# Optimization experiments

Measured on AMD Instinct MI355X. Metric: run time of the kernel, lower is better.

## Reference

```python
import jax, jax.numpy as jnp
import numpy as np

BS, N, D_IN, D_OUT = 4, 512, 64, 64
TEMP = 1.0
POOL_K = 0.5
N_KEEP = max(int(N * POOL_K), 1)  # 256
BN_EPS = 1e-5


def setup_inputs() -> dict:
    key = jax.random.key(0)
    ks = jax.random.split(key, 12)
    xav = lambda k, shape: jax.random.normal(k, shape, jnp.float32) * np.sqrt(2.0 / sum(shape))
    return {
        "x": jax.random.normal(ks[0], (BS, N, D_IN), jnp.float32),
        "att_proj_w": xav(ks[1], (D_IN, D_OUT)),
        "att_proj_b": jnp.zeros((D_OUT,), jnp.float32),
        "att_weight": xav(ks[2], (D_OUT, 1))[:, 0],  # (D_OUT,)
        "pwa_w": xav(ks[3], (D_IN, D_OUT)),
        "pwa_b": jnp.zeros((D_OUT,), jnp.float32),
        "pwoa_w": xav(ks[4], (D_IN, D_OUT)),
        "pwoa_b": jnp.zeros((D_OUT,), jnp.float32),
        "bn_gamma": jnp.ones((D_OUT,), jnp.float32),
        "bn_beta": jnp.zeros((D_OUT,), jnp.float32),
        "bn_mean": jnp.zeros((D_OUT,), jnp.float32),
        "bn_var": jnp.ones((D_OUT,), jnp.float32),
        "pool_w": xav(ks[5], (D_OUT, 1))[:, 0],  # (D_OUT,)
        "pool_b": jnp.zeros((), jnp.float32),
    }


def reference(x, att_proj_w, att_proj_b, att_weight, pwa_w, pwa_b,
              pwoa_w, pwoa_b, bn_gamma, bn_beta, bn_mean, bn_var,
              pool_w, pool_b):
    # ---- GraphAttentionLayer (eval mode: dropout off, BN uses running stats) ----
    # pairwise node product: (bs, i, j, d)
    pair = x[:, :, None, :] * x[:, None, :, :]
    a = jnp.tanh(jnp.einsum('bijd,de->bije', pair, att_proj_w) + att_proj_b)
    scores = jnp.einsum('bije,e->bij', a, att_weight) / TEMP
    att = jax.nn.softmax(scores, axis=-1)  # torch softmax over dim=-2 of (bs,i,j,1) == j axis
    agg = jnp.einsum('bij,bjd->bid', att, x)
    h = (agg @ pwa_w + pwa_b) + (x @ pwoa_w + pwoa_b)
    h = (h - bn_mean) * jax.lax.rsqrt(bn_var + BN_EPS) * bn_gamma + bn_beta
    h = jax.nn.selu(h)
    # ---- GraphPool (eval: dropout off) ----
    s = jax.nn.sigmoid(h @ pool_w + pool_b)  # (bs, N)
    _, idx = jax.lax.top_k(s, N_KEEP)        # (bs, N_KEEP), sorted desc like torch.topk
    hs = h * s[..., None]
    out = jnp.take_along_axis(hs, idx[..., None], axis=1)  # (bs, N_KEEP, D_OUT)
    return out
```

## Files before the change

### kernel.cpp

```cpp
#include <hip/hip_runtime.h>
#include <hip/hip_bf16.h>
#include <math.h>

#define BSZ 4
#define NN 512
#define DD 64
#define NKEEP 256

typedef __attribute__((ext_vector_type(8))) short short8;
typedef __attribute__((ext_vector_type(4))) float f32x4;

__device__ __forceinline__ ushort f2bf_rne(float f) {
  union { float f; unsigned u; } v; v.f = f;
  unsigned r = v.u + 0x7fffu + ((v.u >> 16) & 1u);
  return (ushort)(r >> 16);
}
__device__ __forceinline__ float bf2f(ushort h) {
  union { unsigned u; float f; } v; v.u = ((unsigned)h) << 16;
  return v.f;
}
__device__ __forceinline__ void split2t(float a, float b, uint& hu, uint& lu) {
  const uint au = __float_as_uint(a), bu = __float_as_uint(b);
  hu = (au >> 16) | (bu & 0xffff0000u);
  const float ra = a - __uint_as_float(au & 0xffff0000u);
  const float rb = b - __uint_as_float(bu & 0xffff0000u);
  lu = (__float_as_uint(ra) >> 16) | (__float_as_uint(rb) & 0xffff0000u);
}

__global__ void k_prep(const float* __restrict__ apw,
                       ushort* __restrict__ wht, ushort* __restrict__ wlt,
                       int* __restrict__ tile_tab) {
  const int idx = blockIdx.x * 256 + threadIdx.x;
  const int d = idx >> 6, e = idx & 63;
  const float wv = apw[idx];
  const ushort h = f2bf_rne(wv);
  const ushort lo = f2bf_rne(wv - bf2f(h));
  wht[e * 64 + d] = h;
  wlt[e * 64 + d] = lo;
  if (idx < 1056) {
    int it = 0, rem = idx;
    while (rem >= 32 - (it >> 1)) { rem -= 32 - (it >> 1); ++it; }
    const int jt = (it >> 1) + rem;
    tile_tab[idx] = it | (jt << 8);
  }
}

__global__ __launch_bounds__(256) void k_score(
    const float* __restrict__ x, const ushort* __restrict__ wht,
    const ushort* __restrict__ wlt, const float* __restrict__ apb,
    const float* __restrict__ aw, const int* __restrict__ tile_tab,
    float* __restrict__ sT) {
  __shared__ __align__(16) float T[4][8][16];

  const int w = threadIdx.x >> 6;
  const int l = threadIdx.x & 63;
  const int il = l & 15, g = l >> 4;
  const int task = blockIdx.x * 4 + w;
  const int b = task / 1056;
  const int pid = task - b * 1056;
  const int pk = tile_tab[pid];
  const int it = pk & 0xff, jt = pk >> 8;
  const int i0 = it * 8, j0 = jt * 16;
  const bool diag = ((it >> 1) == jt);

  const float* xb = x + (size_t)b * NN * DD;
  float* plane = sT + (size_t)b * NN * NN;

  short8 wfh[4][2], wfl[4][2];
  #pragma unroll
  for (int eq = 0; eq < 4; ++eq)
    #pragma unroll
    for (int ks = 0; ks < 2; ++ks) {
      const int off = (eq * 16 + il) * 64 + ks * 32 + g * 8;
      wfh[eq][ks] = *reinterpret_cast<const short8*>(wht + off);
      wfl[eq][ks] = *reinterpret_cast<const short8*>(wlt + off);
    }

  const float K2 = 2.8853900817779268f;
  float aw2_4[4], bK2[4], awq = 0.f;
  #pragma unroll
  for (int eq = 0; eq < 4; ++eq) {
    const float a = aw[eq * 16 + il];
    aw2_4[eq] = 2.f * a;
    bK2[eq] = apb[eq * 16 + il] * K2;
    awq += a;
  }
  awq += __shfl_xor(awq, 1, 64);
  awq += __shfl_xor(awq, 2, 64);
  awq += __shfl_xor(awq, 4, 64);
  awq += __shfl_xor(awq, 8, 64);
  const float awC = awq;

  const float* xjr = xb + (size_t)(j0 + il) * DD;
  const float4 xj0 = *reinterpret_cast<const float4*>(xjr + g * 8);
  const float4 xj1 = *reinterpret_cast<const float4*>(xjr + g * 8 + 4);
  const float4 xj2 = *reinterpret_cast<const float4*>(xjr + 32 + g * 8);
  const float4 xj3 = *reinterpret_cast<const float4*>(xjr + 32 + g * 8 + 4);

  const float* xir0 = xb + (size_t)i0 * DD;
  float4 nx0 = *reinterpret_cast<const float4*>(xir0 + g * 8);
  float4 nx1 = *reinterpret_cast<const float4*>(xir0 + g * 8 + 4);
  float4 nx2 = *reinterpret_cast<const float4*>(xir0 + 32 + g * 8);
  float4 nx3 = *reinterpret_cast<const float4*>(xir0 + 32 + g * 8 + 4);

  #pragma unroll 2
  for (int ii = 0; ii < 8; ++ii) {
    const int i_glob = i0 + ii;
    const float4 xi0 = nx0, xi1 = nx1, xi2 = nx2, xi3 = nx3;
    if (ii < 7) {
      const float* xirn = xb + (size_t)(i_glob + 1) * DD;
      nx0 = *reinterpret_cast<const float4*>(xirn + g * 8);
      nx1 = *reinterpret_cast<const float4*>(xirn + g * 8 + 4);
      nx2 = *reinterpret_cast<const float4*>(xirn + 32 + g * 8);
      nx3 = *reinterpret_cast<const float4*>(xirn + 32 + g * 8 + 4);
    }

    union { uint u[4]; short8 s; } hA, lA, hB, lB;
    split2t(xj0.x * xi0.x, xj0.y * xi0.y, hA.u[0], lA.u[0]);
    split2t(xj0.z * xi0.z, xj0.w * xi0.w, hA.u[1], lA.u[1]);
    split2t(xj1.x * xi1.x, xj1.y * xi1.y, hA.u[2], lA.u[2]);
    split2t(xj1.z * xi1.z, xj1.w * xi1.w, hA.u[3], lA.u[3]);
    split2t(xj2.x * xi2.x, xj2.y * xi2.y, hB.u[0], lB.u[0]);
    split2t(xj2.z * xi2.z, xj2.w * xi2.w, hB.u[1], lB.u[1]);
    split2t(xj3.x * xi3.x, xj3.y * xi3.y, hB.u[2], lB.u[2]);
    split2t(xj3.z * xi3.z, xj3.w * xi3.w, hB.u[3], lB.u[3]);

    f32x4 acc[4];
    #pragma unroll
    for (int eq = 0; eq < 4; ++eq) acc[eq] = (f32x4){0.f, 0.f, 0.f, 0.f};
    #pragma unroll
    for (int eq = 0; eq < 4; ++eq) {
      acc[eq] = __builtin_amdgcn_mfma_f32_16x16x32_bf16(hA.s, wfh[eq][0], acc[eq], 0, 0, 0);
      acc[eq] = __builtin_amdgcn_mfma_f32_16x16x32_bf16(hA.s, wfl[eq][0], acc[eq], 0, 0, 0);
      acc[eq] = __builtin_amdgcn_mfma_f32_16x16x32_bf16(lA.s, wfh[eq][0], acc[eq], 0, 0, 0);
      acc[eq] = __builtin_amdgcn_mfma_f32_16x16x32_bf16(hB.s, wfh[eq][1], acc[eq], 0, 0, 0);
      acc[eq] = __builtin_amdgcn_mfma_f32_16x16x32_bf16(hB.s, wfl[eq][1], acc[eq], 0, 0, 0);
      acc[eq] = __builtin_amdgcn_mfma_f32_16x16x32_bf16(lB.s, wfh[eq][1], acc[eq], 0, 0, 0);
    }

    float neg[4] = {0.f, 0.f, 0.f, 0.f};
    #pragma unroll
    for (int eq = 0; eq < 4; ++eq)
      #pragma unroll
      for (int rr = 0; rr < 4; ++rr) {
        const float ex = __builtin_amdgcn_exp2f(fmaf(acc[eq][rr], K2, bK2[eq]));
        const float rc = __builtin_amdgcn_rcpf(ex + 1.0f);
        neg[rr] = fmaf(aw2_4[eq], rc, neg[rr]);
      }
    #pragma unroll
    for (int rr = 0; rr < 4; ++rr) {
      neg[rr] += __shfl_xor(neg[rr], 1, 64);
      neg[rr] += __shfl_xor(neg[rr], 2, 64);
      neg[rr] += __shfl_xor(neg[rr], 4, 64);
      neg[rr] += __shfl_xor(neg[rr], 8, 64);
    }
    const f32x4 sc = {awC - neg[0], awC - neg[1], awC - neg[2], awC - neg[3]};

    if (il == 0) {
      if (!diag) {
        *reinterpret_cast<f32x4*>(plane + (size_t)i_glob * NN + j0 + g * 4) = sc;
      } else {
        #pragma unroll
        for (int rr = 0; rr < 4; ++rr) {
          const int jv = j0 + g * 4 + rr;
          if (jv >= i_glob) plane[(size_t)i_glob * NN + jv] = sc[rr];
        }
      }
      *reinterpret_cast<f32x4*>(&T[w][ii][g * 4]) = sc;
    }
  }

  __syncthreads();

  {
    const int jv = l >> 2;
    const int ip = (l & 3) * 2;
    const float m0 = T[w][ip + 0][jv];
    const float m1 = T[w][ip + 1][jv];
    const int jr = j0 + jv;
    if (!diag) {
      const float2 mv = {m0, m1};
      *reinterpret_cast<float2*>(plane + (size_t)jr * NN + i0 + ip) = mv;
    } else {
      if (jr > i0 + ip + 0) plane[(size_t)jr * NN + i0 + ip + 0] = m0;
      if (jr > i0 + ip + 1) plane[(size_t)jr * NN + i0 + ip + 1] = m1;
    }
  }
}

__global__ __launch_bounds__(256) void k_soft(
    const float* __restrict__ x, const float* __restrict__ sT,
    const float* __restrict__ pwa, const float* __restrict__ pwab,
    const float* __restrict__ pwoa, const float* __restrict__ pwob,
    const float* __restrict__ gam, const float* __restrict__ bet,
    const float* __restrict__ mu, const float* __restrict__ var,
    const float* __restrict__ poolw, const float* __restrict__ poolb,
    float* __restrict__ h, float* __restrict__ s) {
  __shared__ float ssc[2][512];
  __shared__ float srm[2][4], srs[2][4];
  __shared__ float sagg[4][2][64];
  __shared__ float rag[2][64], xis[2][64];

  const int t = threadIdx.x;
  const int w = t >> 6, l = t & 63;
  const int b = blockIdx.x >> 8;
  const int rp = blockIdx.x & 255;
  const int i_r0 = rp * 2, i_r1 = i_r0 + 1;
  const float* xb = x + (size_t)b * NN * DD;
  const float* pl0 = sT + (size_t)b * NN * NN;
  const int jw = w * 128;

  const size_t o0 = (size_t)i_r0 * NN + jw + l;
  const size_t o1 = (size_t)i_r1 * NN + jw + l;
  float r0a = pl0[o0];
  float r0b = pl0[o0 + 64];
  float r1a = pl0[o1];
  float r1b = pl0[o1 + 64];
  float m0 = fmaxf(r0a, r0b), m1 = fmaxf(r1a, r1b);
  #pragma unroll
  for (int off = 32; off; off >>= 1) {
    m0 = fmaxf(m0, __shfl_xor(m0, off, 64));
    m1 = fmaxf(m1, __shfl_xor(m1, off, 64));
  }
  if (l == 0) { srm[0][w] = m0; srm[1][w] = m1; }
  __syncthreads();
  m0 = fmaxf(fmaxf(srm[0][0], srm[0][1]), fmaxf(srm[0][2], srm[0][3]));
  m1 = fmaxf(fmaxf(srm[1][0], srm[1][1]), fmaxf(srm[1][2], srm[1][3]));

  const float L2E = 1.4426950408889634f;
  float e0a = __builtin_amdgcn_exp2f((r0a - m0) * L2E);
  float e0b = __builtin_amdgcn_exp2f((r0b - m0) * L2E);
  float e1a = __builtin_amdgcn_exp2f((r1a - m1) * L2E);
  float e1b = __builtin_amdgcn_exp2f((r1b - m1) * L2E);
  float ps0 = e0a + e0b, ps1 = e1a + e1b;
  #pragma unroll
  for (int off = 32; off; off >>= 1) {
    ps0 += __shfl_xor(ps0, off, 64);
    ps1 += __shfl_xor(ps1, off, 64);
  }
  if (l == 0) { srs[0][w] = ps0; srs[1][w] = ps1; }
  __syncthreads();
  const float inv0 = 1.f / (srs[0][0] + srs[0][1] + srs[0][2] + srs[0][3]);
  const float inv1 = 1.f / (srs[1][0] + srs[1][1] + srs[1][2] + srs[1][3]);
  ssc[0][jw + l] = e0a * inv0;
  ssc[0][jw + 64 + l] = e0b * inv0;
  ssc[1][jw + l] = e1a * inv1;
  ssc[1][jw + 64 + l] = e1b * inv1;
  __syncthreads();

  float g0a = 0.f, g0b = 0.f, g1a = 0.f, g1b = 0.f;
  #pragma unroll 4
  for (int jj = 0; jj < 128; jj += 2) {
    const int j = jw + jj;
    const float xv0 = xb[(size_t)j * DD + l];
    const float xv1 = xb[(size_t)(j + 1) * DD + l];
    g0a = fmaf(ssc[0][j], xv0, g0a);
    g1a = fmaf(ssc[1][j], xv0, g1a);
    g0b = fmaf(ssc[0][j + 1], xv1, g0b);
    g1b = fmaf(ssc[1][j + 1], xv1, g1b);
  }
  sagg[w][0][l] = g0a + g0b;
  sagg[w][1][l] = g1a + g1b;
  __syncthreads();

  if (w < 2) {
    const int irow = i_r0 + w;
    rag[w][l] = sagg[0][w][l] + sagg[1][w][l] + sagg[2][w][l] + sagg[3][w][l];
    xis[w][l] = xb[(size_t)irow * DD + l];
    float acc = 0.f;
    #pragma unroll 8
    for (int d = 0; d < 64; ++d) {
      acc = fmaf(rag[w][d], pwa[d * 64 + l], acc);
      acc = fmaf(xis[w][d], pwoa[d * 64 + l], acc);
    }
    acc += pwab[l] + pwob[l];
    float hb = (acc - mu[l]) * rsqrtf(var[l] + 1e-5f) * gam[l] + bet[l];
    const float SC = 1.0507009873554805f, AL = 1.6732632423543772f;
    float hv = hb > 0.f ? SC * hb : SC * AL * expm1f(hb);
    h[((size_t)(b * NN + irow)) * DD + l] = hv;

    float p = hv * poolw[l];
    #pragma unroll
    for (int off = 32; off; off >>= 1) p += __shfl_xor(p, off, 64);
    if (l == 0) s[b * NN + irow] = 1.f / (1.f + expf(-(p + poolb[0])));
  }
}

__global__ __launch_bounds__(512) void k_sel(
    const float* __restrict__ s, const float* __restrict__ h,
    float* __restrict__ out) {
  __shared__ float svv[NN];
  __shared__ int inv[NKEEP];
  __shared__ float sval[NKEEP];
  const int b = blockIdx.x, t = threadIdx.x;
  svv[t] = s[b * NN + t];
  __syncthreads();

  const float my = svv[t];
  int r = 0;
  #pragma unroll 4
  for (int j0 = 0; j0 < NN; j0 += 4) {
    float4 v = *reinterpret_cast<const float4*>(&svv[j0]);
    r += (v.x > my) || (v.x == my && (j0 + 0) < t);
    r += (v.y > my) || (v.y == my && (j0 + 1) < t);
    r += (v.z > my) || (v.z == my && (j0 + 2) < t);
    r += (v.w > my) || (v.w == my && (j0 + 3) < t);
  }
  if (r < NKEEP) { inv[r] = t; sval[r] = my; }
  __syncthreads();

  #pragma unroll
  for (int pos = t; pos < NKEEP * 16; pos += 512) {
    const int kk = pos >> 4, d4 = (pos & 15) * 4;
    const int i = inv[kk];
    const float sc = sval[kk];
    float4 v = *reinterpret_cast<const float4*>(
        h + ((size_t)(b * NN + i)) * DD + d4);
    v.x *= sc; v.y *= sc; v.z *= sc; v.w *= sc;
    *reinterpret_cast<float4*>(out + ((size_t)(b * NKEEP + kk)) * DD + d4) = v;
  }
}

extern "C" void kernel_launch(void* const* d_in, const int* in_sizes, int n_in,
                              void* d_out, int out_size, void* d_ws, size_t ws_size,
                              hipStream_t stream) {
  const float* x     = (const float*)d_in[0];
  const float* apw   = (const float*)d_in[1];
  const float* apb   = (const float*)d_in[2];
  const float* aw    = (const float*)d_in[3];
  const float* pwa   = (const float*)d_in[4];
  const float* pwab  = (const float*)d_in[5];
  const float* pwoa  = (const float*)d_in[6];
  const float* pwob  = (const float*)d_in[7];
  const float* gam   = (const float*)d_in[8];
  const float* bet   = (const float*)d_in[9];
  const float* mu    = (const float*)d_in[10];
  const float* var   = (const float*)d_in[11];
  const float* poolw = (const float*)d_in[12];
  const float* poolb = (const float*)d_in[13];
  float* out = (float*)d_out;

  float* sT    = (float*)d_ws;
  float* h     = sT + (size_t)BSZ * NN * NN;
  float* s     = h + (size_t)BSZ * NN * DD;
  ushort* wht  = (ushort*)(s + BSZ * NN);
  ushort* wlt  = wht + 4096;
  int* tile_tab = (int*)(wlt + 4096);

  k_prep<<<16, 256, 0, stream>>>(apw, wht, wlt, tile_tab);
  k_score<<<1056, 256, 0, stream>>>(x, wht, wlt, apb, aw, tile_tab, sT);
  k_soft<<<BSZ * 256, 256, 0, stream>>>(x, sT, pwa, pwab, pwoa, pwob,
                                        gam, bet, mu, var, poolw, poolb, h, s);
  k_sel<<<BSZ, 512, 0, stream>>>(s, h, out);
}
```

Before: 73.71 us.

## Fold weight prep into score kernel and make score/softmax kernels persistent

Removes the separate prep kernel: each wave now splits the attention projection weights into bf16 hi/lo fragments itself and derives its triangular tile coordinates inline. Both k_score and k_soft become persistent grids of 512 blocks that loop over tasks. This drops one launch and the workspace round-trip for the prepped weights. In exchange it halves resident parallelism, adds per-wave scalar weight loads and conversion, and removes the next-row x prefetch.

New measurement: 67.02 us. -9.1%, faster.

```diff
diff --git a/kernel.cpp b/kernel.cpp
--- a/kernel.cpp
+++ b/kernel.cpp
@@ -27,53 +27,31 @@
   lu = (__float_as_uint(ra) >> 16) | (__float_as_uint(rb) & 0xffff0000u);
 }
 
-__global__ void k_prep(const float* __restrict__ apw,
-                       ushort* __restrict__ wht, ushort* __restrict__ wlt,
-                       int* __restrict__ tile_tab) {
-  const int idx = blockIdx.x * 256 + threadIdx.x;
-  const int d = idx >> 6, e = idx & 63;
-  const float wv = apw[idx];
-  const ushort h = f2bf_rne(wv);
-  const ushort lo = f2bf_rne(wv - bf2f(h));
-  wht[e * 64 + d] = h;
-  wlt[e * 64 + d] = lo;
-  if (idx < 1056) {
-    int it = 0, rem = idx;
-    while (rem >= 32 - (it >> 1)) { rem -= 32 - (it >> 1); ++it; }
-    const int jt = (it >> 1) + rem;
-    tile_tab[idx] = it | (jt << 8);
-  }
-}
-
 __global__ __launch_bounds__(256) void k_score(
-    const float* __restrict__ x, const ushort* __restrict__ wht,
-    const ushort* __restrict__ wlt, const float* __restrict__ apb,
-    const float* __restrict__ aw, const int* __restrict__ tile_tab,
+    const float* __restrict__ x, const float* __restrict__ apw,
+    const float* __restrict__ apb, const float* __restrict__ aw,
     float* __restrict__ sT) {
   __shared__ __align__(16) float T[4][8][16];
 
   const int w = threadIdx.x >> 6;
   const int l = threadIdx.x & 63;
   const int il = l & 15, g = l >> 4;
-  const int task = blockIdx.x * 4 + w;
-  const int b = task / 1056;
-  const int pid = task - b * 1056;
-  const int pk = tile_tab[pid];
-  const int it = pk & 0xff, jt = pk >> 8;
-  const int i0 = it * 8, j0 = jt * 16;
-  const bool diag = ((it >> 1) == jt);
-
-  const float* xb = x + (size_t)b * NN * DD;
-  float* plane = sT + (size_t)b * NN * NN;
 
   short8 wfh[4][2], wfl[4][2];
   #pragma unroll
   for (int eq = 0; eq < 4; ++eq)
     #pragma unroll
     for (int ks = 0; ks < 2; ++ks) {
-      const int off = (eq * 16 + il) * 64 + ks * 32 + g * 8;
-      wfh[eq][ks] = *reinterpret_cast<const short8*>(wht + off);
-      wfl[eq][ks] = *reinterpret_cast<const short8*>(wlt + off);
+      short8 hh, ll;
+      #pragma unroll
+      for (int q = 0; q < 8; ++q) {
+        const int d = ks * 32 + g * 8 + q;
+        const float wv = apw[d * 64 + eq * 16 + il];
+        const ushort h = f2bf_rne(wv);
+        hh[q] = (short)h;
+        ll[q] = (short)f2bf_rne(wv - bf2f(h));
+      }
+      wfh[eq][ks] = hh; wfl[eq][ks] = ll;
     }
 
   const float K2 = 2.8853900817779268f;
@@ -91,99 +69,103 @@
   awq += __shfl_xor(awq, 8, 64);
   const float awC = awq;
 
-  const float* xjr = xb + (size_t)(j0 + il) * DD;
-  const float4 xj0 = *reinterpret_cast<const float4*>(xjr + g * 8);
-  const float4 xj1 = *reinterpret_cast<const float4*>(xjr + g * 8 + 4);
-  const float4 xj2 = *reinterpret_cast<const float4*>(xjr + 32 + g * 8);
-  const float4 xj3 = *reinterpret_cast<const float4*>(xjr + 32 + g * 8 + 4);
-
-  const float* xir0 = xb + (size_t)i0 * DD;
-  float4 nx0 = *reinterpret_cast<const float4*>(xir0 + g * 8);
-  float4 nx1 = *reinterpret_cast<const float4*>(xir0 + g * 8 + 4);
-  float4 nx2 = *reinterpret_cast<const float4*>(xir0 + 32 + g * 8);
-  float4 nx3 = *reinterpret_cast<const float4*>(xir0 + 32 + g * 8 + 4);
-
-  #pragma unroll 2
-  for (int ii = 0; ii < 8; ++ii) {
-    const int i_glob = i0 + ii;
-    const float4 xi0 = nx0, xi1 = nx1, xi2 = nx2, xi3 = nx3;
-    if (ii < 7) {
-      const float* xirn = xb + (size_t)(i_glob + 1) * DD;
-      nx0 = *reinterpret_cast<const float4*>(xirn + g * 8);
-      nx1 = *reinterpret_cast<const float4*>(xirn + g * 8 + 4);
-      nx2 = *reinterpret_cast<const float4*>(xirn + 32 + g * 8);
-      nx3 = *reinterpret_cast<const float4*>(xirn + 32 + g * 8 + 4);
-    }
-
-    union { uint u[4]; short8 s; } hA, lA, hB, lB;
-    split2t(xj0.x * xi0.x, xj0.y * xi0.y, hA.u[0], lA.u[0]);
-    split2t(xj0.z * xi0.z, xj0.w * xi0.w, hA.u[1], lA.u[1]);
-    split2t(xj1.x * xi1.x, xj1.y * xi1.y, hA.u[2], lA.u[2]);
-    split2t(xj1.z * xi1.z, xj1.w * xi1.w, hA.u[3], lA.u[3]);
-    split2t(xj2.x * xi2.x, xj2.y * xi2.y, hB.u[0], lB.u[0]);
-    split2t(xj2.z * xi2.z, xj2.w * xi2.w, hB.u[1], lB.u[1]);
-    split2t(xj3.x * xi3.x, xj3.y * xi3.y, hB.u[2], lB.u[2]);
-    split2t(xj3.z * xi3.z, xj3.w * xi3.w, hB.u[3], lB.u[3]);
-
-    f32x4 acc[4];
-    #pragma unroll
-    for (int eq = 0; eq < 4; ++eq) acc[eq] = (f32x4){0.f, 0.f, 0.f, 0.f};
-    #pragma unroll
-    for (int eq = 0; eq < 4; ++eq) {
-      acc[eq] = __builtin_amdgcn_mfma_f32_16x16x32_bf16(hA.s, wfh[eq][0], acc[eq], 0, 0, 0);
-      acc[eq] = __builtin_amdgcn_mfma_f32_16x16x32_bf16(hA.s, wfl[eq][0], acc[eq], 0, 0, 0);
-      acc[eq] = __builtin_amdgcn_mfma_f32_16x16x32_bf16(lA.s, wfh[eq][0], acc[eq], 0, 0, 0);
-      acc[eq] = __builtin_amdgcn_mfma_f32_16x16x32_bf16(hB.s, wfh[eq][1], acc[eq], 0, 0, 0);
-      acc[eq] = __builtin_amdgcn_mfma_f32_16x16x32_bf16(hB.s, wfl[eq][1], acc[eq], 0, 0, 0);
-      acc[eq] = __builtin_amdgcn_mfma_f32_16x16x32_bf16(lB.s, wfh[eq][1], acc[eq], 0, 0, 0);
-    }
-
-    float neg[4] = {0.f, 0.f, 0.f, 0.f};
-    #pragma unroll
-    for (int eq = 0; eq < 4; ++eq)
-      #pragma unroll
-      for (int rr = 0; rr < 4; ++rr) {
-        const float ex = __builtin_amdgcn_exp2f(fmaf(acc[eq][rr], K2, bK2[eq]));
-        const float rc = __builtin_amdgcn_rcpf(ex + 1.0f);
-        neg[rr] = fmaf(aw2_4[eq], rc, neg[rr]);
-      }
-    #pragma unroll
-    for (int rr = 0; rr < 4; ++rr) {
-      neg[rr] += __shfl_xor(neg[rr], 1, 64);
-      neg[rr] += __shfl_xor(neg[rr], 2, 64);
-      neg[rr] += __shfl_xor(neg[rr], 4, 64);
-      neg[rr] += __shfl_xor(neg[rr], 8, 64);
-    }
-    const f32x4 sc = {awC - neg[0], awC - neg[1], awC - neg[2], awC - neg[3]};
-
-    if (il == 0) {
-      if (!diag) {
-        *reinterpret_cast<f32x4*>(plane + (size_t)i_glob * NN + j0 + g * 4) = sc;
-      } else {
+  const int wave_id = blockIdx.x * 4 + w;
+
+  for (int task = wave_id; task < 4224; task += 2048) {
+    const int b = task / 1056;
+    const int pid = task - b * 1056;
+    int it = 0, rem = pid;
+    while (rem >= 32 - (it >> 1)) { rem -= 32 - (it >> 1); ++it; }
+    const int jt = (it >> 1) + rem;
+    const int i0 = it * 8, j0 = jt * 16;
+    const bool diag = ((it >> 1) == jt);
+
+    const float* xb = x + (size_t)b * NN * DD;
+    float* plane = sT + (size_t)b * NN * NN;
+
+    const float* xjr = xb + (size_t)(j0 + il) * DD;
+    const float4 xj0 = *reinterpret_cast<const float4*>(xjr + g * 8);
+    const float4 xj1 = *reinterpret_cast<const float4*>(xjr + g * 8 + 4);
+    const float4 xj2 = *reinterpret_cast<const float4*>(xjr + 32 + g * 8);
+    const float4 xj3 = *reinterpret_cast<const float4*>(xjr + 32 + g * 8 + 4);
+
+    #pragma unroll 2
+    for (int ii = 0; ii < 8; ++ii) {
+      const int i_glob = i0 + ii;
+      const float* xir = xb + (size_t)i_glob * DD;
+      const float4 xi0 = *reinterpret_cast<const float4*>(xir + g * 8);
+      const float4 xi1 = *reinterpret_cast<const float4*>(xir + g * 8 + 4);
+      const float4 xi2 = *reinterpret_cast<const float4*>(xir + 32 + g * 8);
+      const float4 xi3 = *reinterpret_cast<const float4*>(xir + 32 + g * 8 + 4);
+
+      union { uint u[4]; short8 s; } hA, lA, hB, lB;
+      split2t(xj0.x * xi0.x, xj0.y * xi0.y, hA.u[0], lA.u[0]);
+      split2t(xj0.z * xi0.z, xj0.w * xi0.w, hA.u[1], lA.u[1]);
+      split2t(xj1.x * xi1.x, xj1.y * xi1.y, hA.u[2], lA.u[2]);
+      split2t(xj1.z * xi1.z, xj1.w * xi1.w, hA.u[3], lA.u[3]);
+      split2t(xj2.x * xi2.x, xj2.y * xi2.y, hB.u[0], lB.u[0]);
+      split2t(xj2.z * xi2.z, xj2.w * xi2.w, hB.u[1], lB.u[1]);
+      split2t(xj3.x * xi3.x, xj3.y * xi3.y, hB.u[2], lB.u[2]);
+      split2t(xj3.z * xi3.z, xj3.w * xi3.w, hB.u[3], lB.u[3]);
+
+      f32x4 acc[4];
+      #pragma unroll
+      for (int eq = 0; eq < 4; ++eq) acc[eq] = (f32x4){0.f, 0.f, 0.f, 0.f};
+      #pragma unroll
+      for (int eq = 0; eq < 4; ++eq) {
+        acc[eq] = __builtin_amdgcn_mfma_f32_16x16x32_bf16(hA.s, wfh[eq][0], acc[eq], 0, 0, 0);
+        acc[eq] = __builtin_amdgcn_mfma_f32_16x16x32_bf16(hA.s, wfl[eq][0], acc[eq], 0, 0, 0);
+        acc[eq] = __builtin_amdgcn_mfma_f32_16x16x32_bf16(lA.s, wfh[eq][0], acc[eq], 0, 0, 0);
+        acc[eq] = __builtin_amdgcn_mfma_f32_16x16x32_bf16(hB.s, wfh[eq][1], acc[eq], 0, 0, 0);
+        acc[eq] = __builtin_amdgcn_mfma_f32_16x16x32_bf16(hB.s, wfl[eq][1], acc[eq], 0, 0, 0);
+        acc[eq] = __builtin_amdgcn_mfma_f32_16x16x32_bf16(lB.s, wfh[eq][1], acc[eq], 0, 0, 0);
+      }
+
+      float neg[4] = {0.f, 0.f, 0.f, 0.f};
+      #pragma unroll
+      for (int eq = 0; eq < 4; ++eq)
         #pragma unroll
         for (int rr = 0; rr < 4; ++rr) {
-          const int jv = j0 + g * 4 + rr;
-          if (jv >= i_glob) plane[(size_t)i_glob * NN + jv] = sc[rr];
+          const float ex = __builtin_amdgcn_exp2f(fmaf(acc[eq][rr], K2, bK2[eq]));
+          const float rc = __builtin_amdgcn_rcpf(ex + 1.0f);
+          neg[rr] = fmaf(aw2_4[eq], rc, neg[rr]);
         }
-      }
-      *reinterpret_cast<f32x4*>(&T[w][ii][g * 4]) = sc;
-    }
-  }
-
-  __syncthreads();
-
-  {
-    const int jv = l >> 2;
-    const int ip = (l & 3) * 2;
-    const float m0 = T[w][ip + 0][jv];
-    const float m1 = T[w][ip + 1][jv];
-    const int jr = j0 + jv;
-    if (!diag) {
-      const float2 mv = {m0, m1};
-      *reinterpret_cast<float2*>(plane + (size_t)jr * NN + i0 + ip) = mv;
-    } else {
-      if (jr > i0 + ip + 0) plane[(size_t)jr * NN + i0 + ip + 0] = m0;
-      if (jr > i0 + ip + 1) plane[(size_t)jr * NN + i0 + ip + 1] = m1;
+      #pragma unroll
+      for (int rr = 0; rr < 4; ++rr) {
+        neg[rr] += __shfl_xor(neg[rr], 1, 64);
+        neg[rr] += __shfl_xor(neg[rr], 2, 64);
+        neg[rr] += __shfl_xor(neg[rr], 4, 64);
+        neg[rr] += __shfl_xor(neg[rr], 8, 64);
+      }
+      const f32x4 sc = {awC - neg[0], awC - neg[1], awC - neg[2], awC - neg[3]};
+
+      if (il == 0) {
+        if (!diag) {
+          *reinterpret_cast<f32x4*>(plane + (size_t)i_glob * NN + j0 + g * 4) = sc;
+        } else {
+          #pragma unroll
+          for (int rr = 0; rr < 4; ++rr) {
+            const int jv = j0 + g * 4 + rr;
+            if (jv >= i_glob) plane[(size_t)i_glob * NN + jv] = sc[rr];
+          }
+        }
+        *reinterpret_cast<f32x4*>(&T[w][ii][g * 4]) = sc;
+      }
+    }
+
+    {
+      const int jv = l >> 2;
+      const int ip = (l & 3) * 2;
+      const float m0 = T[w][ip + 0][jv];
+      const float m1 = T[w][ip + 1][jv];
+      const int jr = j0 + jv;
+      if (!diag) {
+        const float2 mv = {m0, m1};
+        *reinterpret_cast<float2*>(plane + (size_t)jr * NN + i0 + ip) = mv;
+      } else {
+        if (jr > i0 + ip + 0) plane[(size_t)jr * NN + i0 + ip + 0] = m0;
+        if (jr > i0 + ip + 1) plane[(size_t)jr * NN + i0 + ip + 1] = m1;
+      }
     }
   }
 }
@@ -203,86 +185,90 @@
 
   const int t = threadIdx.x;
   const int w = t >> 6, l = t & 63;
-  const int b = blockIdx.x >> 8;
-  const int rp = blockIdx.x & 255;
-  const int i_r0 = rp * 2, i_r1 = i_r0 + 1;
-  const float* xb = x + (size_t)b * NN * DD;
-  const float* pl0 = sT + (size_t)b * NN * NN;
   const int jw = w * 128;
 
-  const size_t o0 = (size_t)i_r0 * NN + jw + l;
-  const size_t o1 = (size_t)i_r1 * NN + jw + l;
-  float r0a = pl0[o0];
-  float r0b = pl0[o0 + 64];
-  float r1a = pl0[o1];
-  float r1b = pl0[o1 + 64];
-  float m0 = fmaxf(r0a, r0b), m1 = fmaxf(r1a, r1b);
-  #pragma unroll
-  for (int off = 32; off; off >>= 1) {
-    m0 = fmaxf(m0, __shfl_xor(m0, off, 64));
-    m1 = fmaxf(m1, __shfl_xor(m1, off, 64));
-  }
-  if (l == 0) { srm[0][w] = m0; srm[1][w] = m1; }
-  __syncthreads();
-  m0 = fmaxf(fmaxf(srm[0][0], srm[0][1]), fmaxf(srm[0][2], srm[0][3]));
-  m1 = fmaxf(fmaxf(srm[1][0], srm[1][1]), fmaxf(srm[1][2], srm[1][3]));
-
-  const float L2E = 1.4426950408889634f;
-  float e0a = __builtin_amdgcn_exp2f((r0a - m0) * L2E);
-  float e0b = __builtin_amdgcn_exp2f((r0b - m0) * L2E);
-  float e1a = __builtin_amdgcn_exp2f((r1a - m1) * L2E);
-  float e1b = __builtin_amdgcn_exp2f((r1b - m1) * L2E);
-  float ps0 = e0a + e0b, ps1 = e1a + e1b;
-  #pragma unroll
-  for (int off = 32; off; off >>= 1) {
-    ps0 += __shfl_xor(ps0, off, 64);
-    ps1 += __shfl_xor(ps1, off, 64);
-  }
-  if (l == 0) { srs[0][w] = ps0; srs[1][w] = ps1; }
-  __syncthreads();
-  const float inv0 = 1.f / (srs[0][0] + srs[0][1] + srs[0][2] + srs[0][3]);
-  const float inv1 = 1.f / (srs[1][0] + srs[1][1] + srs[1][2] + srs[1][3]);
-  ssc[0][jw + l] = e0a * inv0;
-  ssc[0][jw + 64 + l] = e0b * inv0;
-  ssc[1][jw + l] = e1a * inv1;
-  ssc[1][jw + 64 + l] = e1b * inv1;
-  __syncthreads();
-
-  float g0a = 0.f, g0b = 0.f, g1a = 0.f, g1b = 0.f;
-  #pragma unroll 4
-  for (int jj = 0; jj < 128; jj += 2) {
-    const int j = jw + jj;
-    const float xv0 = xb[(size_t)j * DD + l];
-    const float xv1 = xb[(size_t)(j + 1) * DD + l];
-    g0a = fmaf(ssc[0][j], xv0, g0a);
-    g1a = fmaf(ssc[1][j], xv0, g1a);
-    g0b = fmaf(ssc[0][j + 1], xv1, g0b);
-    g1b = fmaf(ssc[1][j + 1], xv1, g1b);
-  }
-  sagg[w][0][l] = g0a + g0b;
-  sagg[w][1][l] = g1a + g1b;
-  __syncthreads();
-
-  if (w < 2) {
-    const int irow = i_r0 + w;
-    rag[w][l] = sagg[0][w][l] + sagg[1][w][l] + sagg[2][w][l] + sagg[3][w][l];
-    xis[w][l] = xb[(size_t)irow * DD + l];
-    float acc = 0.f;
-    #pragma unroll 8
-    for (int d = 0; d < 64; ++d) {
-      acc = fmaf(rag[w][d], pwa[d * 64 + l], acc);
-      acc = fmaf(xis[w][d], pwoa[d * 64 + l], acc);
-    }
-    acc += pwab[l] + pwob[l];
-    float hb = (acc - mu[l]) * rsqrtf(var[l] + 1e-5f) * gam[l] + bet[l];
-    const float SC = 1.0507009873554805f, AL = 1.6732632423543772f;
-    float hv = hb > 0.f ? SC * hb : SC * AL * expm1f(hb);
-    h[((size_t)(b * NN + irow)) * DD + l] = hv;
-
-    float p = hv * poolw[l];
+  for (int task = blockIdx.x; task < 1024; task += 512) {
+    const int b = task >> 8;
+    const int rp = task & 255;
+    const int i_r0 = rp * 2, i_r1 = i_r0 + 1;
+    const float* xb = x + (size_t)b * NN * DD;
+    const float* pl0 = sT + (size_t)b * NN * NN;
+
+    const size_t o0 = (size_t)i_r0 * NN + jw + l;
+    const size_t o1 = (size_t)i_r1 * NN + jw + l;
+    float r0a = pl0[o0];
+    float r0b = pl0[o0 + 64];
+    float r1a = pl0[o1];
+    float r1b = pl0[o1 + 64];
+    float m0 = fmaxf(r0a, r0b), m1 = fmaxf(r1a, r1b);
     #pragma unroll
-    for (int off = 32; off; off >>= 1) p += __shfl_xor(p, off, 64);
-    if (l == 0) s[b * NN + irow] = 1.f / (1.f + expf(-(p + poolb[0])));
+    for (int off = 32; off; off >>= 1) {
+      m0 = fmaxf(m0, __shfl_xor(m0, off, 64));
+      m1 = fmaxf(m1, __shfl_xor(m1, off, 64));
+    }
+    if (l == 0) { srm[0][w] = m0; srm[1][w] = m1; }
+    __syncthreads();
+    m0 = fmaxf(fmaxf(srm[0][0], srm[0][1]), fmaxf(srm[0][2], srm[0][3]));
+    m1 = fmaxf(fmaxf(srm[1][0], srm[1][1]), fmaxf(srm[1][2], srm[1][3]));
+
+    const float L2E = 1.4426950408889634f;
+    float e0a = __builtin_amdgcn_exp2f((r0a - m0) * L2E);
+    float e0b = __builtin_amdgcn_exp2f((r0b - m0) * L2E);
+    float e1a = __builtin_amdgcn_exp2f((r1a - m1) * L2E);
+    float e1b = __builtin_amdgcn_exp2f((r1b - m1) * L2E);
+    float ps0 = e0a + e0b, ps1 = e1a + e1b;
+    #pragma unroll
+    for (int off = 32; off; off >>= 1) {
+      ps0 += __shfl_xor(ps0, off, 64);
+      ps1 += __shfl_xor(ps1, off, 64);
+    }
+    if (l == 0) { srs[0][w] = ps0; srs[1][w] = ps1; }
+    __syncthreads();
+    const float inv0 = 1.f / (srs[0][0] + srs[0][1] + srs[0][2] + srs[0][3]);
+    const float inv1 = 1.f / (srs[1][0] + srs[1][1] + srs[1][2] + srs[1][3]);
+    ssc[0][jw + l] = e0a * inv0;
+    ssc[0][jw + 64 + l] = e0b * inv0;
+    ssc[1][jw + l] = e1a * inv1;
+    ssc[1][jw + 64 + l] = e1b * inv1;
+    __syncthreads();
+
+    float g0a = 0.f, g0b = 0.f, g1a = 0.f, g1b = 0.f;
+    #pragma unroll 4
+    for (int jj = 0; jj < 128; jj += 2) {
+      const int j = jw + jj;
+      const float xv0 = xb[(size_t)j * DD + l];
+      const float xv1 = xb[(size_t)(j + 1) * DD + l];
+      g0a = fmaf(ssc[0][j], xv0, g0a);
+      g1a = fmaf(ssc[1][j], xv0, g1a);
+      g0b = fmaf(ssc[0][j + 1], xv1, g0b);
+      g1b = fmaf(ssc[1][j + 1], xv1, g1b);
+    }
+    sagg[w][0][l] = g0a + g0b;
+    sagg[w][1][l] = g1a + g1b;
+    __syncthreads();
+
+    if (w < 2) {
+      const int irow = i_r0 + w;
+      rag[w][l] = sagg[0][w][l] + sagg[1][w][l] + sagg[2][w][l] + sagg[3][w][l];
+      xis[w][l] = xb[(size_t)irow * DD + l];
+      float acc = 0.f;
+      #pragma unroll 8
+      for (int d = 0; d < 64; ++d) {
+        acc = fmaf(rag[w][d], pwa[d * 64 + l], acc);
+        acc = fmaf(xis[w][d], pwoa[d * 64 + l], acc);
+      }
+      acc += pwab[l] + pwob[l];
+      float hb = (acc - mu[l]) * rsqrtf(var[l] + 1e-5f) * gam[l] + bet[l];
+      const float SC = 1.0507009873554805f, AL = 1.6732632423543772f;
+      float hv = hb > 0.f ? SC * hb : SC * AL * expm1f(hb);
+      h[((size_t)(b * NN + irow)) * DD + l] = hv;
+
+      float p = hv * poolw[l];
+      #pragma unroll
+      for (int off = 32; off; off >>= 1) p += __shfl_xor(p, off, 64);
+      if (l == 0) s[b * NN + irow] = 1.f / (1.f + expf(-(p + poolb[0])));
+    }
+    __syncthreads();
   }
 }
 
@@ -340,16 +326,12 @@
   const float* poolb = (const float*)d_in[13];
   float* out = (float*)d_out;
 
-  float* sT    = (float*)d_ws;
-  float* h     = sT + (size_t)BSZ * NN * NN;
-  float* s     = h + (size_t)BSZ * NN * DD;
-  ushort* wht  = (ushort*)(s + BSZ * NN);
-  ushort* wlt  = wht + 4096;
-  int* tile_tab = (int*)(wlt + 4096);
-
-  k_prep<<<16, 256, 0, stream>>>(apw, wht, wlt, tile_tab);
-  k_score<<<1056, 256, 0, stream>>>(x, wht, wlt, apb, aw, tile_tab, sT);
-  k_soft<<<BSZ * 256, 256, 0, stream>>>(x, sT, pwa, pwab, pwoa, pwob,
-                                        gam, bet, mu, var, poolw, poolb, h, s);
+  float* sT = (float*)d_ws;
+  float* h  = sT + (size_t)BSZ * NN * NN;
+  float* s  = h + (size_t)BSZ * NN * DD;
+
+  k_score<<<512, 256, 0, stream>>>(x, apw, apb, aw, sT);
+  k_soft<<<512, 256, 0, stream>>>(x, sT, pwa, pwab, pwoa, pwob,
+                                  gam, bet, mu, var, poolw, poolb, h, s);
   k_sel<<<BSZ, 512, 0, stream>>>(s, h, out);
 }
```
